# Performance work log

Measured on AMD Instinct MI355X. Metric: run time of the kernel, lower is better.

Reference implementation:

```python
import jax, jax.numpy as jnp
import numpy as np

BATCH = 4096
NUM_CLASSES = 10000
FEAT_DIM = 512


def setup_inputs() -> dict:
    key = jax.random.key(0)
    k1, k2, k3 = jax.random.split(key, 3)
    x = jax.random.normal(k1, (BATCH, FEAT_DIM), dtype=jnp.float32)
    labels = jax.random.randint(k2, (BATCH,), 0, NUM_CLASSES)
    centers = jax.random.normal(k3, (NUM_CLASSES, FEAT_DIM), dtype=jnp.float32)
    lr = jnp.array([0.1], dtype=jnp.float32)
    return {"x": x, "labels": labels, "centers": centers, "lr": lr}


def reference(x, labels, centers, lr):
    batch, feat_dim = x.shape
    n_classes = centers.shape[0]

    # --- center update (vectorized replacement of the per-class/per-sample double loop) ---
    # A_j = count_j * centers[j] - sum_{i: label_i==j} x_i ;  delta_j = A_j / (1 + count_j)
    ones = jnp.ones((batch,), dtype=x.dtype)
    counts = jax.ops.segment_sum(ones, labels, num_segments=n_classes)          # [C]
    sum_x = jax.ops.segment_sum(x, labels, num_segments=n_classes)              # [C, D]
    delta = (counts[:, None] * centers - sum_x) / (1.0 + counts[:, None])       # [C, D]
    # torch wraps the result in a fresh nn.Parameter -> detached from autograd graph
    centers_new = jax.lax.stop_gradient(centers - lr[0] * delta)

    # --- pairwise squared distances, then 1/(1+d) ---
    d = (jnp.sum(x * x, axis=1, keepdims=True)                                   # [B, 1]
         + jnp.sum(centers_new * centers_new, axis=1)[None, :]                   # [1, C]
         - 2.0 * (x @ centers_new.T))                                            # [B, C]
    d = 1.0 / (1.0 + d)

    # --- masked reduction: row sum minus the own-class entry, clamped ---
    row_sum = d.sum(axis=1)                                                      # [B]
    own = jnp.take_along_axis(d, labels[:, None], axis=1)[:, 0]                  # [B]
    dist = jnp.clip(row_sum - own, 1e-12, 1e12)
    return dist.mean()
```

## Files before the change

kernel.cpp:

```cpp
#include <hip/hip_runtime.h>
#include <hip/hip_bf16.h>

#define BATCH 4096
#define NCLS  10000
#define CPAD  10240
#define FDIM  512
#define MAXL  32

typedef float f32x4 __attribute__((ext_vector_type(4)));
typedef int   ix4   __attribute__((ext_vector_type(4)));
typedef int   ix8   __attribute__((ext_vector_type(8)));

__device__ static inline void gld_lds16(const void* g, void* l) {
    __builtin_amdgcn_global_load_lds(
        (const __attribute__((address_space(1))) void*)g,
        (__attribute__((address_space(3))) void*)l, 16, 0, 0);
}

__device__ static inline unsigned int fp4e(float v) {
    unsigned int s = (__float_as_uint(v) >> 31) << 3;
    float a = fabsf(v);
    unsigned int c;
    if      (a < 1.25f) c = (a < 0.75f) ? (a < 0.25f ? 0u : 1u) : 2u;
    else if (a < 2.5f)  c = (a < 1.75f) ? 3u : 4u;
    else                c = (a < 3.5f) ? 5u : (a < 5.f ? 6u : 7u);
    return s | c;
}

__device__ static inline int pdst4(int row, int k) {
    return (row >> 4) * 4096 + (k >> 7) * 1024
         + ((k >> 5) & 3) * 256 + (row & 15) * 16 + ((k & 31) >> 1);
}

__global__ void prep_all(const float* __restrict__ x, const int* __restrict__ labels,
                         const float* __restrict__ centers, const float* __restrict__ lr,
                         unsigned char* __restrict__ xq, float* __restrict__ xnorm,
                         unsigned char* __restrict__ cq, float* __restrict__ cnorm,
                         float* __restrict__ out) {
    const int bid = blockIdx.x, t = threadIdx.x;
    __shared__ float red[4];
    if (bid < BATCH) {
        if (bid == 0 && t == 0) out[0] = 0.f;
        int i = bid;
        float2 v = *(const float2*)&x[(size_t)i * FDIM + 2 * t];
        xq[pdst4(i, 2 * t)] = (unsigned char)(fp4e(v.x) | (fp4e(v.y) << 4));
        float s = v.x * v.x + v.y * v.y;
#pragma unroll
        for (int m = 1; m < 64; m <<= 1) s += __shfl_xor(s, m);
        if ((t & 63) == 0) red[t >> 6] = s;
        __syncthreads();
        if (t == 0) xnorm[i] = red[0] + red[1] + red[2] + red[3];
        return;
    }
    int j = bid - BATCH;
    if (j >= NCLS) {
        cq[pdst4(j, 2 * t)] = 0;
        if (t == 0) cnorm[j] = 1e30f;
        return;
    }
    __shared__ int nmatch;
    __shared__ int idxs[MAXL];
    if (t == 0) nmatch = 0;
    __syncthreads();
    {
        const int4* l4 = (const int4*)labels;
        int4 a0 = l4[t], a1 = l4[t + 256], a2 = l4[t + 512], a3 = l4[t + 768];
#define CHK(V, B) { \
        if (V.x == j) { int p = atomicAdd(&nmatch, 1); if (p < MAXL) idxs[p] = (B); } \
        if (V.y == j) { int p = atomicAdd(&nmatch, 1); if (p < MAXL) idxs[p] = (B) + 1; } \
        if (V.z == j) { int p = atomicAdd(&nmatch, 1); if (p < MAXL) idxs[p] = (B) + 2; } \
        if (V.w == j) { int p = atomicAdd(&nmatch, 1); if (p < MAXL) idxs[p] = (B) + 3; } }
        CHK(a0, 4 * t) CHK(a1, 4 * (t + 256)) CHK(a2, 4 * (t + 512)) CHK(a3, 4 * (t + 768))
#undef CHK
    }
    __syncthreads();
    int cfull = nmatch;
    int c = cfull > MAXL ? MAXL : cfull;
    if (t == 0 && c > 1) {
        for (int a = 1; a < c; ++a) {
            int v = idxs[a]; int b = a - 1;
            while (b >= 0 && idxs[b] > v) { idxs[b + 1] = idxs[b]; --b; }
            idxs[b + 1] = v;
        }
    }
    __syncthreads();
    float cf  = (float)cfull;
    float lr0 = lr[0];
    float inv = 1.f / (1.f + cf);
    float c0 = centers[(size_t)j * FDIM + 2 * t];
    float c1 = centers[(size_t)j * FDIM + 2 * t + 1];
    float sx0 = 0.f, sx1 = 0.f;
    for (int q = 0; q < c; ++q) {
        const float* xr = &x[(size_t)idxs[q] * FDIM + 2 * t];
        sx0 += xr[0]; sx1 += xr[1];
    }
    float n0 = c0 - lr0 * (cf * c0 - sx0) * inv;
    float n1 = c1 - lr0 * (cf * c1 - sx1) * inv;
    cq[pdst4(j, 2 * t)] = (unsigned char)(fp4e(n0) | (fp4e(n1) << 4));
    float cn2 = n0 * n0 + n1 * n1;
#pragma unroll
    for (int m = 1; m < 64; m <<= 1) cn2 += __shfl_xor(cn2, m);
    if ((t & 63) == 0) red[t >> 6] = cn2;
    __syncthreads();
    if (t == 0) cnorm[j] = red[0] + red[1] + red[2] + red[3];
}

__global__ void __launch_bounds__(256, 2)
pairwise(const unsigned char* __restrict__ xq, const unsigned char* __restrict__ cq,
         const float* __restrict__ xnorm, const float* __restrict__ cnorm,
         const int* __restrict__ labels, float* __restrict__ row_part) {
    __shared__ unsigned char Als[32768];
    __shared__ unsigned char Bls[32768];
    const int tid = threadIdx.x;
    const int w = tid >> 6, lane = tid & 63;
    const int lr16 = lane & 15, lhi = lane >> 4;
    const int bid = blockIdx.x;
    const int swz = (bid & 7) * 320 + (bid >> 3);
    const int bx = swz & 31, by = swz >> 5;
    const int m_blk = bx * 128, n_blk = by * 128;
    const int mq = (w >> 1) * 64, nq = (w & 1) * 64;

    f32x4 acc[4][4];
#pragma unroll
    for (int a = 0; a < 4; ++a)
#pragma unroll
        for (int b = 0; b < 4; ++b) acc[a][b] = (f32x4)0.f;

    const unsigned char* gA = xq + (size_t)(m_blk >> 4) * 4096 + tid * 16;
    const unsigned char* gB = cq + (size_t)(n_blk >> 4) * 4096 + tid * 16;
#pragma unroll
    for (int q = 0; q < 8; ++q) {
        gld_lds16(gA + q * 4096, &Als[q * 4096 + tid * 16]);
        gld_lds16(gB + q * 4096, &Bls[q * 4096 + tid * 16]);
    }
    asm volatile("s_waitcnt vmcnt(0)" ::: "memory");
    __builtin_amdgcn_s_barrier();

#pragma unroll
    for (int kt2 = 0; kt2 < 4; ++kt2) {
        ix8 af[4], bg[4];
#pragma unroll
        for (int mi = 0; mi < 4; ++mi) {
            ix4 lo = *(const ix4*)&Als[((mq >> 4) + mi) * 4096 + kt2 * 1024 + lane * 16];
            af[mi] = __builtin_shufflevector(lo, lo, 0, 1, 2, 3, 0, 1, 2, 3);
        }
#pragma unroll
        for (int ni = 0; ni < 4; ++ni) {
            ix4 lo = *(const ix4*)&Bls[((nq >> 4) + ni) * 4096 + kt2 * 1024 + lane * 16];
            bg[ni] = __builtin_shufflevector(lo, lo, 0, 1, 2, 3, 0, 1, 2, 3);
        }
        __builtin_amdgcn_s_setprio(1);
#pragma unroll
        for (int mi = 0; mi < 4; ++mi)
#pragma unroll
            for (int ni = 0; ni < 4; ++ni)
                acc[mi][ni] = __builtin_amdgcn_mfma_scale_f32_16x16x128_f8f6f4(
                    bg[ni], af[mi], acc[mi][ni], 4, 4, 0, 0x7F7F7F7F, 0, 0x7F7F7F7F);
        __builtin_amdgcn_s_setprio(0);
    }

    float rsum[4];
#pragma unroll
    for (int mi = 0; mi < 4; ++mi) {
        int m_g = m_blk + mq + mi * 16 + lr16;
        float xn1 = 1.f + xnorm[m_g];
        int lab = labels[m_g];
        float s = 0.f;
#pragma unroll
        for (int ni = 0; ni < 4; ++ni) {
#pragma unroll
            for (int r = 0; r < 4; ++r) {
                int n_g = n_blk + nq + ni * 16 + lhi * 4 + r;
                float d1 = xn1 + cnorm[n_g] - 2.f * acc[mi][ni][r];
                float rc = __builtin_amdgcn_rcpf(d1);
                s += (n_g != lab) ? rc : 0.f;
            }
        }
        s += __shfl_xor(s, 16);
        s += __shfl_xor(s, 32);
        rsum[mi] = s;
    }
    __syncthreads();
    float* spart = (float*)&Als[0];
    if ((w & 1) && lhi == 0) {
#pragma unroll
        for (int mi = 0; mi < 4; ++mi)
            spart[mq + mi * 16 + lr16] = rsum[mi];
    }
    __syncthreads();
    if (!(w & 1) && lhi == 0) {
        float* rp = row_part + (size_t)by * BATCH + m_blk;
#pragma unroll
        for (int mi = 0; mi < 4; ++mi) {
            int ml = mq + mi * 16 + lr16;
            rp[ml] = rsum[mi] + spart[ml];
        }
    }
}

__global__ void finalize(const float* __restrict__ row_part, float* __restrict__ out) {
    int i = blockIdx.x * 256 + threadIdx.x;
    float s = 0.f;
    for (int p = 0; p < CPAD / 128; ++p) s += row_part[(size_t)p * BATCH + i];
    float dist = fminf(fmaxf(s, 1e-12f), 1e12f);
    float v = dist * (1.f / BATCH);
#pragma unroll
    for (int m = 1; m < 64; m <<= 1) v += __shfl_xor(v, m);
    __shared__ float red[4];
    if ((threadIdx.x & 63) == 0) red[threadIdx.x >> 6] = v;
    __syncthreads();
    if (threadIdx.x == 0) atomicAdd(out, red[0] + red[1] + red[2] + red[3]);
}

extern "C" void kernel_launch(void* const* d_in, const int* in_sizes, int n_in,
                              void* d_out, int out_size, void* d_ws, size_t ws_size,
                              hipStream_t stream) {
    const float* x       = (const float*)d_in[0];
    const int*   labels  = (const int*)d_in[1];
    const float* centers = (const float*)d_in[2];
    const float* lr      = (const float*)d_in[3];
    float* out = (float*)d_out;

    char* ws = (char*)d_ws;
    size_t off = 0;
    unsigned char* cq = (unsigned char*)(ws + off); off += (size_t)CPAD * FDIM / 2;
    unsigned char* xq = (unsigned char*)(ws + off); off += (size_t)BATCH * FDIM / 2;
    float* cnorm    = (float*)(ws + off); off += (size_t)CPAD * 4;
    float* xnorm    = (float*)(ws + off); off += (size_t)BATCH * 4;
    float* row_part = (float*)(ws + off); off += (size_t)(CPAD / 128) * BATCH * 4;

    prep_all<<<BATCH + CPAD, 256, 0, stream>>>(x, labels, centers, lr,
                                               xq, xnorm, cq, cnorm, out);
    pairwise<<<(BATCH / 128) * (CPAD / 128), 256, 0, stream>>>(xq, cq, xnorm, cnorm, labels, row_part);
    finalize<<<BATCH / 256, 256, 0, stream>>>(row_part, out);
}
```

Before: 47.44 us.

## Make pairwise blocks persistent over class groups with double-buffered B tiles

```diff
diff --git a/kernel.cpp b/kernel.cpp
--- a/kernel.cpp
+++ b/kernel.cpp
@@ -110,78 +110,113 @@
          const float* __restrict__ xnorm, const float* __restrict__ cnorm,
          const int* __restrict__ labels, float* __restrict__ row_part) {
     __shared__ unsigned char Als[32768];
-    __shared__ unsigned char Bls[32768];
+    __shared__ unsigned char Bls[2][16384];
+    __shared__ unsigned char Cnls[4096];
     const int tid = threadIdx.x;
     const int w = tid >> 6, lane = tid & 63;
     const int lr16 = lane & 15, lhi = lane >> 4;
     const int bid = blockIdx.x;
-    const int swz = (bid & 7) * 320 + (bid >> 3);
-    const int bx = swz & 31, by = swz >> 5;
-    const int m_blk = bx * 128, n_blk = by * 128;
-    const int mq = (w >> 1) * 64, nq = (w & 1) * 64;
-
-    f32x4 acc[4][4];
-#pragma unroll
-    for (int a = 0; a < 4; ++a)
-#pragma unroll
-        for (int b = 0; b < 4; ++b) acc[a][b] = (f32x4)0.f;
-
-    const unsigned char* gA = xq + (size_t)(m_blk >> 4) * 4096 + tid * 16;
-    const unsigned char* gB = cq + (size_t)(n_blk >> 4) * 4096 + tid * 16;
-#pragma unroll
-    for (int q = 0; q < 8; ++q) {
-        gld_lds16(gA + q * 4096, &Als[q * 4096 + tid * 16]);
-        gld_lds16(gB + q * 4096, &Bls[q * 4096 + tid * 16]);
-    }
-    asm volatile("s_waitcnt vmcnt(0)" ::: "memory");
-    __builtin_amdgcn_s_barrier();
-
-#pragma unroll
-    for (int kt2 = 0; kt2 < 4; ++kt2) {
-        ix8 af[4], bg[4];
-#pragma unroll
-        for (int mi = 0; mi < 4; ++mi) {
-            ix4 lo = *(const ix4*)&Als[((mq >> 4) + mi) * 4096 + kt2 * 1024 + lane * 16];
-            af[mi] = __builtin_shufflevector(lo, lo, 0, 1, 2, 3, 0, 1, 2, 3);
-        }
-#pragma unroll
-        for (int ni = 0; ni < 4; ++ni) {
-            ix4 lo = *(const ix4*)&Bls[((nq >> 4) + ni) * 4096 + kt2 * 1024 + lane * 16];
-            bg[ni] = __builtin_shufflevector(lo, lo, 0, 1, 2, 3, 0, 1, 2, 3);
-        }
-        __builtin_amdgcn_s_setprio(1);
-#pragma unroll
-        for (int mi = 0; mi < 4; ++mi)
-#pragma unroll
-            for (int ni = 0; ni < 4; ++ni)
-                acc[mi][ni] = __builtin_amdgcn_mfma_scale_f32_16x16x128_f8f6f4(
-                    bg[ni], af[mi], acc[mi][ni], 4, 4, 0, 0x7F7F7F7F, 0, 0x7F7F7F7F);
-        __builtin_amdgcn_s_setprio(0);
-    }
-
-    float rsum[4];
+    const int swz = (bid & 7) * 64 + (bid >> 3);
+    const int bx = swz & 31, g = swz >> 5;
+    const int m_blk = bx * 128;
+    const int mq = (w >> 1) * 64, nqh = (w & 1) * 32;
+
+    float xn[4]; int lab[4];
 #pragma unroll
     for (int mi = 0; mi < 4; ++mi) {
         int m_g = m_blk + mq + mi * 16 + lr16;
-        float xn1 = 1.f + xnorm[m_g];
-        int lab = labels[m_g];
-        float s = 0.f;
-#pragma unroll
-        for (int ni = 0; ni < 4; ++ni) {
+        xn[mi]  = xnorm[m_g];
+        lab[mi] = labels[m_g];
+    }
+    {
+        const unsigned char* gA = xq + (size_t)(m_blk >> 4) * 4096 + tid * 16;
+#pragma unroll
+        for (int q = 0; q < 8; ++q) gld_lds16(gA + q * 4096, &Als[q * 4096 + tid * 16]);
+        gld_lds16((const char*)cnorm + (size_t)g * 2560 + tid * 16, &Cnls[tid * 16]);
+        const unsigned char* gB0 = cq + (size_t)g * 40960 + tid * 16;
+#pragma unroll
+        for (int q = 0; q < 4; ++q) gld_lds16(gB0 + q * 4096, &Bls[0][q * 4096 + tid * 16]);
+    }
+    const unsigned char* gB = cq + (size_t)g * 40960 + tid * 16;
+
+    ix8 afr[4][4];
+    f32x4 acc[4][2];
+    float rsum[4] = {0.f, 0.f, 0.f, 0.f};
+
+    for (int s = 0; s < 10; ++s) {
+        if (s < 9) {
+            const unsigned char* gs = gB + (size_t)(s + 1) * 16384;
+            unsigned char* ls = &Bls[(s + 1) & 1][0];
+#pragma unroll
+            for (int q = 0; q < 4; ++q) gld_lds16(gs + q * 4096, &ls[q * 4096 + tid * 16]);
+            asm volatile("s_waitcnt vmcnt(4)" ::: "memory");
+        } else {
+            asm volatile("s_waitcnt vmcnt(0)" ::: "memory");
+        }
+        __builtin_amdgcn_s_barrier();
+
+        if (s == 0) {
+#pragma unroll
+            for (int mi = 0; mi < 4; ++mi)
+#pragma unroll
+                for (int kt2 = 0; kt2 < 4; ++kt2) {
+                    ix4 lo = *(const ix4*)&Als[((mq >> 4) + mi) * 4096 + kt2 * 1024 + lane * 16];
+                    afr[mi][kt2] = __builtin_shufflevector(lo, lo, 0, 1, 2, 3, 0, 1, 2, 3);
+                }
+        }
+
+#pragma unroll
+        for (int mi = 0; mi < 4; ++mi)
+#pragma unroll
+            for (int ni = 0; ni < 2; ++ni) acc[mi][ni] = (f32x4)0.f;
+
+        const unsigned char* bb = &Bls[s & 1][0];
+#pragma unroll
+        for (int kt2 = 0; kt2 < 4; ++kt2) {
+            ix8 bg[2];
+#pragma unroll
+            for (int ni = 0; ni < 2; ++ni) {
+                ix4 lo = *(const ix4*)&bb[((nqh >> 4) + ni) * 4096 + kt2 * 1024 + lane * 16];
+                bg[ni] = __builtin_shufflevector(lo, lo, 0, 1, 2, 3, 0, 1, 2, 3);
+            }
+            __builtin_amdgcn_s_setprio(1);
+#pragma unroll
+            for (int mi = 0; mi < 4; ++mi)
+#pragma unroll
+                for (int ni = 0; ni < 2; ++ni)
+                    acc[mi][ni] = __builtin_amdgcn_mfma_scale_f32_16x16x128_f8f6f4(
+                        bg[ni], afr[mi][kt2], acc[mi][ni], 4, 4, 0, 0x7F7F7F7F, 0, 0x7F7F7F7F);
+            __builtin_amdgcn_s_setprio(0);
+        }
+        __builtin_amdgcn_sched_barrier(0);
+        __builtin_amdgcn_s_barrier();
+
+        const float* cnf = (const float*)&Cnls[0];
+        int nb_l = s * 64 + nqh;
+        int nb_g = g * 640 + nb_l;
+#pragma unroll
+        for (int ni = 0; ni < 2; ++ni) {
 #pragma unroll
             for (int r = 0; r < 4; ++r) {
-                int n_g = n_blk + nq + ni * 16 + lhi * 4 + r;
-                float d1 = xn1 + cnorm[n_g] - 2.f * acc[mi][ni][r];
-                float rc = __builtin_amdgcn_rcpf(d1);
-                s += (n_g != lab) ? rc : 0.f;
+                float cn = cnf[nb_l + ni * 16 + lhi * 4 + r];
+                int n_g = nb_g + ni * 16 + lhi * 4 + r;
+#pragma unroll
+                for (int mi = 0; mi < 4; ++mi) {
+                    float d1 = 1.f + xn[mi] + cn - 2.f * acc[mi][ni][r];
+                    float rc = __builtin_amdgcn_rcpf(d1);
+                    rsum[mi] += (n_g != lab[mi]) ? rc : 0.f;
+                }
             }
         }
-        s += __shfl_xor(s, 16);
-        s += __shfl_xor(s, 32);
-        rsum[mi] = s;
-    }
-    __syncthreads();
-    float* spart = (float*)&Als[0];
+    }
+
+#pragma unroll
+    for (int mi = 0; mi < 4; ++mi) {
+        rsum[mi] += __shfl_xor(rsum[mi], 16);
+        rsum[mi] += __shfl_xor(rsum[mi], 32);
+    }
+    __syncthreads();
+    float* spart = (float*)&Bls[0][0];
     if ((w & 1) && lhi == 0) {
 #pragma unroll
         for (int mi = 0; mi < 4; ++mi)
@@ -189,7 +224,7 @@
     }
     __syncthreads();
     if (!(w & 1) && lhi == 0) {
-        float* rp = row_part + (size_t)by * BATCH + m_blk;
+        float* rp = row_part + (size_t)g * BATCH + m_blk;
 #pragma unroll
         for (int mi = 0; mi < 4; ++mi) {
             int ml = mq + mi * 16 + lr16;
@@ -201,7 +236,8 @@
 __global__ void finalize(const float* __restrict__ row_part, float* __restrict__ out) {
     int i = blockIdx.x * 256 + threadIdx.x;
     float s = 0.f;
-    for (int p = 0; p < CPAD / 128; ++p) s += row_part[(size_t)p * BATCH + i];
+#pragma unroll
+    for (int p = 0; p < 16; ++p) s += row_part[(size_t)p * BATCH + i];
     float dist = fminf(fmaxf(s, 1e-12f), 1e12f);
     float v = dist * (1.f / BATCH);
 #pragma unroll
@@ -227,10 +263,10 @@
     unsigned char* xq = (unsigned char*)(ws + off); off += (size_t)BATCH * FDIM / 2;
     float* cnorm    = (float*)(ws + off); off += (size_t)CPAD * 4;
     float* xnorm    = (float*)(ws + off); off += (size_t)BATCH * 4;
-    float* row_part = (float*)(ws + off); off += (size_t)(CPAD / 128) * BATCH * 4;
+    float* row_part = (float*)(ws + off); off += (size_t)16 * BATCH * 4;
 
     prep_all<<<BATCH + CPAD, 256, 0, stream>>>(x, labels, centers, lr,
                                                xq, xnorm, cq, cnorm, out);
-    pairwise<<<(BATCH / 128) * (CPAD / 128), 256, 0, stream>>>(xq, cq, xnorm, cnorm, labels, row_part);
+    pairwise<<<512, 256, 0, stream>>>(xq, cq, xnorm, cnorm, labels, row_part);
     finalize<<<BATCH / 256, 256, 0, stream>>>(row_part, out);
 }
```

Result: faster. 43.60 us (-8.1%).
